# Performance work log

Measured on AMD Instinct MI355X. Metric: run time of the kernel, lower is better.

The kernel has to match this reference:

```python
import jax, jax.numpy as jnp
import numpy as np

J = 17  # coco joints
SKEL = ((1, 2), (0, 1), (0, 2), (2, 4), (1, 3), (6, 8), (8, 10), (5, 7), (7, 9),
        (12, 14), (14, 16), (11, 13), (13, 15), (5, 6), (11, 12), (5, 11), (6, 12), (3, 5), (4, 6))
EPS = 1e-5


def make_adj():
    a = np.eye(J, dtype=np.float32)
    for i, j in SKEL:
        a[i, j] = 1.0
        a[j, i] = 1.0
    return jnp.asarray(a)


def conv_block(feat, W, b, g, be, adj):
    # feat: [B,V,Din], W: [V,Din,Dout], b/g/be: [V,Dout]
    h = jnp.einsum('bvd,vdo->bvo', feat, W) + b
    # BatchNorm1d (training mode): per-vertex, per-channel batch stats (biased var)
    mu = h.mean(axis=0)
    var = h.var(axis=0)
    h = (h - mu) * jax.lax.rsqrt(var + EPS) * g + be
    h = jnp.einsum('vu,buo->bvo', adj, h)  # adjacency aggregation
    return jax.nn.relu(h)


def setup_inputs() -> dict:
    key = jax.random.key(0)
    ks = jax.random.split(key, 10)
    B, Din = 8192, 2048
    s0 = 1.0 / np.sqrt(Din)
    s1 = 1.0 / np.sqrt(J)
    img_feat = jax.random.normal(ks[0], (B, J, Din), dtype=jnp.float32)
    # first GraphConvBlock: 2048 -> 17, per-vertex params
    W0 = jax.random.uniform(ks[1], (J, Din, J), jnp.float32, -s0, s0)
    b0 = jax.random.uniform(ks[2], (J, J), jnp.float32, -s0, s0)
    g0 = jnp.ones((J, J), jnp.float32)
    be0 = jnp.zeros((J, J), jnp.float32)
    # 4 GraphResBlocks x 2 GraphConvBlocks = 8 blocks of dim 17 -> 17
    Wr = jax.random.uniform(ks[3], (8, J, J, J), jnp.float32, -s1, s1)
    br = jax.random.uniform(ks[4], (8, J, J), jnp.float32, -s1, s1)
    gr = jnp.ones((8, J, J), jnp.float32)
    ber = jnp.zeros((8, J, J), jnp.float32)
    return {"img_feat": img_feat, "W0": W0, "b0": b0, "g0": g0, "be0": be0,
            "Wr": Wr, "br": br, "gr": gr, "ber": ber}


def reference(img_feat, W0, b0, g0, be0, Wr, br, gr, ber):
    adj = make_adj()
    feat = conv_block(img_feat, W0, b0, g0, be0, adj)  # [B,17,17]
    for r in range(4):  # 4 GraphResBlocks
        i0, i1 = 2 * r, 2 * r + 1
        h = conv_block(feat, Wr[i0], br[i0], gr[i0], ber[i0], adj)
        h = conv_block(h, Wr[i1], br[i1], gr[i1], ber[i1], adj)
        feat = h + feat  # residual
    return feat
```

## Files before the change

kernel.cpp:

```cpp
#include <hip/hip_runtime.h>

#define J 17
#define JP 18
#define VO 289
#define NB 8192
#define DIN 2048
#define EPSB 1e-5f
#define KC 512
#define RT 32
#define NCH 68

typedef __attribute__((ext_vector_type(8))) short bf16x8;
typedef __attribute__((ext_vector_type(4))) float f32x4;
typedef __attribute__((ext_vector_type(4))) float f32x4v;

__device__ __constant__ unsigned ADJM[J] = {
  0x7u, 0xFu, 0x17u, 0x2Au, 0x54u, 0x8E8u, 0x1170u, 0x2A0u, 0x540u,
  0x280u, 0x500u, 0x3820u, 0x5840u, 0xA800u, 0x15000u, 0xA000u, 0x14000u};

__device__ inline unsigned short f2bf(float x){
  unsigned u = __float_as_uint(x);
  return (unsigned short)((u + 0x7fffu + ((u>>16)&1u)) >> 16);
}

__global__ void zero_stats(float* p, int n) {
  int i = blockIdx.x*blockDim.x + threadIdx.x;
  int stride = gridDim.x*blockDim.x;
  for (; i < n; i += stride) p[i] = 0.f;
}

__global__ __launch_bounds__(256) void wconv_kernel(
    const float* __restrict__ W0, unsigned short* __restrict__ Wp)
{
  int t = blockIdx.x*256 + threadIdx.x;
  int v = t >> 11, k = t & 2047;
  const float* src = W0 + (size_t)t*J;
  unsigned short* dst = Wp + (((size_t)v*256 + (k>>3))*17)*8 + (k&7);
  #pragma unroll
  for (int o=0;o<J;++o)  dst[o*8] = f2bf(src[o]);
}

__global__ __launch_bounds__(512) void conv0_kernel(
    const float* __restrict__ feat, const unsigned short* __restrict__ Wp,
    const float* __restrict__ b0, float* __restrict__ C,
    float* __restrict__ stat0)
{
  const int tid = threadIdx.x, w = tid>>6, l = tid&63;
  const int lo = l&15, oc = l>>4;
  const int sr = tid>>4, sc = tid&15;
  const int rowBase = blockIdx.x*RT;

  __shared__ __align__(16) unsigned short Ab[2][RT*KC];
  __shared__ float red[8][2][256];
  __shared__ float bS[VO], bQ[VO];

  for (int i=tid;i<VO;i+=512){ bS[i]=0.f; bQ[i]=0.f; }

  f32x4 acc00 = (f32x4){0.f,0.f,0.f,0.f};
  f32x4 acc01 = (f32x4){0.f,0.f,0.f,0.f};
  f32x4 acc10 = (f32x4){0.f,0.f,0.f,0.f};
  f32x4 acc11 = (f32x4){0.f,0.f,0.f,0.f};

  const float* frow = feat + (size_t)(rowBase + sr)*(J*DIN);
  f32x4v ld[8];

  auto issue = [&](int c){
    const f32x4v* src = (const f32x4v*)(frow + c*KC + sc*4);
    #pragma unroll
    for (int i=0;i<8;++i) ld[i] = __builtin_nontemporal_load(src + i*16);
  };
  auto writeLDS = [&](int buf){
    #pragma unroll
    for (int i=0;i<8;++i){
      ushort4 hv;
      hv.x=f2bf(ld[i].x); hv.y=f2bf(ld[i].y); hv.z=f2bf(ld[i].z); hv.w=f2bf(ld[i].w);
      const int f = sc*4 + i*64;
      *(ushort4*)&Ab[buf][(sr*KC + f) ^ ((sr&7)<<3)] = hv;
    }
  };

  issue(0); writeLDS(0);
  __syncthreads();

  const int swz = (lo&7)<<3;

  for (int c=0;c<NCH;++c){
    const int buf = c&1;
    if (c+1<NCH) issue(c+1);
    const int v = c>>2;
    #pragma unroll
    for (int ks=0;ks<2;++ks){
      const int kl = w*64 + ks*32 + oc*8;
      bf16x8 a0 = *(const bf16x8*)&Ab[buf][(lo*KC + kl) ^ swz];
      bf16x8 a1 = *(const bf16x8*)&Ab[buf][((16+lo)*KC + kl) ^ swz];
      const int kg8 = ((c&3)*KC + kl) >> 3;
      const unsigned short* fragBase = Wp + (((size_t)v*256 + kg8)*17)*8;
      bf16x8 bA = *(const bf16x8*)(fragBase + lo*8);
      bf16x8 bB = {0,0,0,0,0,0,0,0};
      if (lo==0) bB = *(const bf16x8*)(fragBase + 16*8);
      acc00 = __builtin_amdgcn_mfma_f32_16x16x32_bf16(a0, bA, acc00, 0,0,0);
      acc10 = __builtin_amdgcn_mfma_f32_16x16x32_bf16(a1, bA, acc10, 0,0,0);
      acc01 = __builtin_amdgcn_mfma_f32_16x16x32_bf16(a0, bB, acc01, 0,0,0);
      acc11 = __builtin_amdgcn_mfma_f32_16x16x32_bf16(a1, bB, acc11, 0,0,0);
    }
    if ((c&3)==3){
      #pragma unroll
      for (int pass=0; pass<2; ++pass){
        #pragma unroll
        for (int r=0;r<4;++r){
          red[w][0][(oc*4+r)*16+lo] = pass ? acc10[r] : acc00[r];
          red[w][1][(oc*4+r)*16+lo] = pass ? acc11[r] : acc01[r];
        }
        __syncthreads();
        if (tid < 256){
          const int er = tid>>4, ec = tid&15;
          const int ri = er*16+ec;
          float h0 = red[0][0][ri]+red[1][0][ri]+red[2][0][ri]+red[3][0][ri]
                   + red[4][0][ri]+red[5][0][ri]+red[6][0][ri]+red[7][0][ri]
                   + b0[v*J+ec];
          const int row = rowBase + pass*16 + er;
          C[(size_t)row*VO + v*J + ec] = h0;
          float s0 = h0, q0 = h0*h0;
          float s1 = 0.f, q1 = 0.f;
          if (ec==0){
            const int r2 = er*16;
            float h1 = red[0][1][r2]+red[1][1][r2]+red[2][1][r2]+red[3][1][r2]
                     + red[4][1][r2]+red[5][1][r2]+red[6][1][r2]+red[7][1][r2]
                     + b0[v*J+16];
            C[(size_t)row*VO + v*J + 16] = h1;
            s1 = h1; q1 = h1*h1;
          }
          s0 += __shfl_xor(s0,16); s0 += __shfl_xor(s0,32);
          q0 += __shfl_xor(q0,16); q0 += __shfl_xor(q0,32);
          s1 += __shfl_xor(s1,16); s1 += __shfl_xor(s1,32);
          q1 += __shfl_xor(q1,16); q1 += __shfl_xor(q1,32);
          if (l < 16){ atomicAdd(&bS[v*J+l], s0); atomicAdd(&bQ[v*J+l], q0); }
          if (l == 0){ atomicAdd(&bS[v*J+16], s1); atomicAdd(&bQ[v*J+16], q1); }
        }
        __syncthreads();
      }
      acc00 = (f32x4){0.f,0.f,0.f,0.f};
      acc01 = (f32x4){0.f,0.f,0.f,0.f};
      acc10 = (f32x4){0.f,0.f,0.f,0.f};
      acc11 = (f32x4){0.f,0.f,0.f,0.f};
    }
    if (c+1<NCH){
      writeLDS(buf^1);
      __syncthreads();
    }
  }

  __syncthreads();
  const int rep = blockIdx.x & 7;
  for (int i=tid;i<VO;i+=512){
    atomicAdd(&stat0[rep*512+i],        bS[i]);
    atomicAdd(&stat0[4096 + rep*512+i], bQ[i]);
  }
}

template<int RESID,int WRITEF,int CONV>
__global__ __launch_bounds__(256) void chain_kernel(
  const float* __restrict__ Cin, float* __restrict__ Cout,
  float* __restrict__ F,
  const float* __restrict__ statJ,
  const float* __restrict__ g, const float* __restrict__ be,
  const float* __restrict__ Wc, const float* __restrict__ bc,
  float* __restrict__ statN)
{
  __shared__ float wsmT[J*J*JP];
  __shared__ float bb[VO];
  __shared__ float aC[VO], cC[VO];
  __shared__ float hbX[4][2][J*JP];
  __shared__ float ssum[VO], ssq[VO];
  const int tid = threadIdx.x, wv = tid>>6, lane = tid&63;

  if (CONV) {
    for (int i=tid;i<J*J*J;i+=256) {
      int v = i/VO, rem = i - v*VO, d = rem/J, o = rem - d*J;
      wsmT[(v*J+o)*JP + d] = Wc[i];
    }
    for (int i=tid;i<VO;i+=256) bb[i]=bc[i];
  }
  for (int i=tid;i<VO;i+=256) {
    float s=0.f,q=0.f;
    #pragma unroll
    for (int r=0;r<8;++r){ s += statJ[r*512+i]; q += statJ[4096 + r*512+i]; }
    float mu  = s*(1.f/NB);
    float var = q*(1.f/NB) - mu*mu;
    float rs  = rsqrtf(var + EPSB);
    float A = rs*g[i];
    aC[i]=A; cC[i]=be[i]-mu*A;
    ssum[i]=0.f; ssq[i]=0.f;
  }
  __syncthreads();

  float sl[5]={0,0,0,0,0}, ql[5]={0,0,0,0,0};

  #pragma unroll
  for (int it=0; it<2; ++it) {
    const int r0 = blockIdx.x*16 + wv*4 + it*2;
    const float* c0 = Cin + (size_t)r0*VO;
    const float* c1 = c0 + VO;

    #pragma unroll
    for (int s=0;s<5;++s) {
      int vo = lane + 64*s;
      if (vo<VO) {
        int vtx = vo/J, o = vo - vtx*J;
        hbX[wv][0][vtx*JP+o] = c0[vo]*aC[vo] + cC[vo];
        hbX[wv][1][vtx*JP+o] = c1[vo]*aC[vo] + cC[vo];
      }
    }
    asm volatile("s_waitcnt lgkmcnt(0)" ::: "memory");

    float n0[5], n1[5];
    #pragma unroll
    for (int s=0;s<5;++s) {
      int vo = lane + 64*s;
      n0[s]=0.f; n1[s]=0.f;
      if (vo<VO) {
        int vtx = vo/J, o = vo - vtx*J;
        unsigned m = ADJM[vtx];
        float a0=0.f, a1=0.f;
        while (m) {
          int u = __ffs(m) - 1; m &= m-1;
          a0 += hbX[wv][0][u*JP+o];
          a1 += hbX[wv][1][u*JP+o];
        }
        a0 = a0>0.f?a0:0.f; a1 = a1>0.f?a1:0.f;
        size_t gi = (size_t)r0*VO + vo;
        if (RESID)  { a0 += F[gi]; a1 += F[gi+VO]; }
        if (WRITEF) { F[gi]=a0;    F[gi+VO]=a1; }
        n0[s]=a0; n1[s]=a1;
        if (!CONV) { Cout[gi]=a0; Cout[gi+VO]=a1; }
      }
    }

    if (CONV) {
      #pragma unroll
      for (int s=0;s<5;++s) {
        int vo = lane + 64*s;
        if (vo<VO) {
          int vtx = vo/J, o = vo - vtx*J;
          hbX[wv][0][vtx*JP+o] = n0[s];
          hbX[wv][1][vtx*JP+o] = n1[s];
        }
      }
      asm volatile("s_waitcnt lgkmcnt(0)" ::: "memory");
      #pragma unroll
      for (int s=0;s<5;++s) {
        int vo = lane + 64*s;
        if (vo<VO) {
          int vtx = vo/J, o = vo - vtx*J;
          const float* wp = &wsmT[(vtx*J+o)*JP];
          const float* h0 = &hbX[wv][0][vtx*JP];
          const float* h1 = &hbX[wv][1][vtx*JP];
          float a0 = bb[vo], a1 = a0;
          #pragma unroll
          for (int d=0;d<J;++d) {
            float w = wp[d];
            a0 += h0[d]*w; a1 += h1[d]*w;
          }
          size_t gi = (size_t)r0*VO + vo;
          Cout[gi]=a0; Cout[gi+VO]=a1;
          sl[s] += a0+a1; ql[s] += a0*a0 + a1*a1;
        }
      }
      asm volatile("s_waitcnt lgkmcnt(0)" ::: "memory");
    } else {
      asm volatile("s_waitcnt lgkmcnt(0)" ::: "memory");
    }
  }

  if (CONV) {
    #pragma unroll
    for (int s=0;s<5;++s) {
      int vo = lane + 64*s;
      if (vo<VO) { atomicAdd(&ssum[vo], sl[s]); atomicAdd(&ssq[vo], ql[s]); }
    }
    __syncthreads();
    const int rep = blockIdx.x & 7;
    for (int i=tid;i<VO;i+=256) {
      atomicAdd(&statN[rep*512+i],        ssum[i]);
      atomicAdd(&statN[4096 + rep*512+i], ssq[i]);
    }
  }
}

extern "C" void kernel_launch(void* const* d_in, const int* in_sizes, int n_in,
                              void* d_out, int out_size, void* d_ws, size_t ws_size,
                              hipStream_t stream)
{
  (void)in_sizes; (void)n_in; (void)out_size; (void)ws_size;
  const float* img = (const float*)d_in[0];
  const float* W0  = (const float*)d_in[1];
  const float* b0  = (const float*)d_in[2];
  const float* g0  = (const float*)d_in[3];
  const float* be0 = (const float*)d_in[4];
  const float* Wr  = (const float*)d_in[5];
  const float* br  = (const float*)d_in[6];
  const float* gr  = (const float*)d_in[7];
  const float* ber = (const float*)d_in[8];

  float* ws = (float*)d_ws;
  float* ST = ws;
  unsigned short* Wp = (unsigned short*)(ws + 73728);
  float* Ca = ws + 73728 + 300000;
  float* Cb = Ca + (size_t)NB*VO;
  float* F  = Cb + (size_t)NB*VO;
  float* out = (float*)d_out;

  zero_stats<<<72,256,0,stream>>>(ST, 9*8192);
  wconv_kernel<<<136,256,0,stream>>>(W0, Wp);

  conv0_kernel<<<256,512,0,stream>>>(img, Wp, b0, Ca, ST);

  const int W1 = J*J*J;
  #define STG(j) (ST + (j)*8192)
  chain_kernel<0,1,1><<<512,256,0,stream>>>(Ca, Cb, F, STG(0), g0,      be0,
                                            Wr+0*W1, br+0*VO, STG(1));
  chain_kernel<0,0,1><<<512,256,0,stream>>>(Cb, Ca, F, STG(1), gr+0*VO, ber+0*VO,
                                            Wr+1*W1, br+1*VO, STG(2));
  chain_kernel<1,1,1><<<512,256,0,stream>>>(Ca, Cb, F, STG(2), gr+1*VO, ber+1*VO,
                                            Wr+2*W1, br+2*VO, STG(3));
  chain_kernel<0,0,1><<<512,256,0,stream>>>(Cb, Ca, F, STG(3), gr+2*VO, ber+2*VO,
                                            Wr+3*W1, br+3*VO, STG(4));
  chain_kernel<1,1,1><<<512,256,0,stream>>>(Ca, Cb, F, STG(4), gr+3*VO, ber+3*VO,
                                            Wr+4*W1, br+4*VO, STG(5));
  chain_kernel<0,0,1><<<512,256,0,stream>>>(Cb, Ca, F, STG(5), gr+4*VO, ber+4*VO,
                                            Wr+5*W1, br+5*VO, STG(6));
  chain_kernel<1,1,1><<<512,256,0,stream>>>(Ca, Cb, F, STG(6), gr+5*VO, ber+5*VO,
                                            Wr+6*W1, br+6*VO, STG(7));
  chain_kernel<0,0,1><<<512,256,0,stream>>>(Cb, Ca, F, STG(7), gr+6*VO, ber+6*VO,
                                            Wr+7*W1, br+7*VO, STG(8));
  chain_kernel<1,0,0><<<512,256,0,stream>>>(Ca, out, F, STG(8), gr+7*VO, ber+7*VO,
                                            nullptr, nullptr, nullptr);
  #undef STG
}
```

Before: 431.3 us.

## Use bf16 MFMA for per-vertex 17x17 residual convs in chain kernel

Replaces the scalar fp32 per-vertex 17x17 matmul in the chain kernel with bf16 MFMA 16x16x32 instructions. The 16 rows of a block are staged as bf16 in a swizzled LDS buffer, and the weights are pre-packed into fragment layouts, with a second MFMA covering the 17th output channel. The intent is to cut the ALU cost of the small dense contractions and the per-row LDS traffic. In exchange, the residual-block activations and weights are rounded to bf16, which adds precision error, and most lanes of the second MFMA do wasted work.

```diff
diff --git a/kernel.cpp b/kernel.cpp
--- a/kernel.cpp
+++ b/kernel.cpp
@@ -167,123 +167,121 @@
   const float* __restrict__ Wc, const float* __restrict__ bc,
   float* __restrict__ statN)
 {
-  __shared__ float wsmT[J*J*JP];
-  __shared__ float bb[VO];
-  __shared__ float aC[VO], cC[VO];
-  __shared__ float hbX[4][2][J*JP];
+  __shared__ float aC[VO], cC[VO], bb[VO];
   __shared__ float ssum[VO], ssq[VO];
+  __shared__ float hb1[4][4][J*JP];
+  __shared__ __align__(16) unsigned short hb2[16*576];
+  __shared__ __align__(16) unsigned short wfA[17][64][8];
+  __shared__ __align__(16) unsigned short wfB[17][4][8];
+
   const int tid = threadIdx.x, wv = tid>>6, lane = tid&63;
-
-  if (CONV) {
-    for (int i=tid;i<J*J*J;i+=256) {
-      int v = i/VO, rem = i - v*VO, d = rem/J, o = rem - d*J;
-      wsmT[(v*J+o)*JP + d] = Wc[i];
-    }
-    for (int i=tid;i<VO;i+=256) bb[i]=bc[i];
-  }
-  for (int i=tid;i<VO;i+=256) {
+  const int lo = lane&15, oc = lane>>4;
+  const int rowBase = blockIdx.x*16;
+
+  for (int i=tid;i<VO;i+=256){
     float s=0.f,q=0.f;
     #pragma unroll
     for (int r=0;r<8;++r){ s += statJ[r*512+i]; q += statJ[4096 + r*512+i]; }
     float mu  = s*(1.f/NB);
     float var = q*(1.f/NB) - mu*mu;
-    float rs  = rsqrtf(var + EPSB);
-    float A = rs*g[i];
+    float A = rsqrtf(var + EPSB)*g[i];
     aC[i]=A; cC[i]=be[i]-mu*A;
     ssum[i]=0.f; ssq[i]=0.f;
-  }
-  __syncthreads();
-
-  float sl[5]={0,0,0,0,0}, ql[5]={0,0,0,0,0};
+    if (CONV) bb[i]=bc[i];
+  }
+  if (CONV){
+    for (int i=tid;i<16*576/8;i+=256) ((uint4*)hb2)[i] = (uint4){0,0,0,0};
+    for (int idx=tid; idx<17*64; idx+=256){
+      int v=idx>>6, ll=idx&63, c=ll&15, o8=ll>>4;
+      unsigned short* dst=&wfA[v][ll][0];
+      #pragma unroll
+      for (int j=0;j<8;++j){ int d=o8*8+j; dst[j] = (d<J)? f2bf(Wc[((size_t)v*J+d)*J+c]) : (unsigned short)0; }
+    }
+    for (int idx=tid; idx<17*4; idx+=256){
+      int v=idx>>2, o8=idx&3;
+      unsigned short* dst=&wfB[v][o8][0];
+      #pragma unroll
+      for (int j=0;j<8;++j){ int d=o8*8+j; dst[j] = (d<J)? f2bf(Wc[((size_t)v*J+d)*J+16]) : (unsigned short)0; }
+    }
+  }
+  __syncthreads();
 
   #pragma unroll
-  for (int it=0; it<2; ++it) {
-    const int r0 = blockIdx.x*16 + wv*4 + it*2;
-    const float* c0 = Cin + (size_t)r0*VO;
-    const float* c1 = c0 + VO;
-
-    #pragma unroll
-    for (int s=0;s<5;++s) {
+  for (int r4=0;r4<4;++r4){
+    const int row = wv*4 + r4;
+    const float* cr = Cin + (size_t)(rowBase+row)*VO;
+    #pragma unroll
+    for (int s=0;s<5;++s){
       int vo = lane + 64*s;
-      if (vo<VO) {
-        int vtx = vo/J, o = vo - vtx*J;
-        hbX[wv][0][vtx*JP+o] = c0[vo]*aC[vo] + cC[vo];
-        hbX[wv][1][vtx*JP+o] = c1[vo]*aC[vo] + cC[vo];
-      }
-    }
-    asm volatile("s_waitcnt lgkmcnt(0)" ::: "memory");
-
-    float n0[5], n1[5];
-    #pragma unroll
-    for (int s=0;s<5;++s) {
+      if (vo<VO){ int vtx=vo/J, o=vo-vtx*J; hb1[wv][r4][vtx*JP+o] = cr[vo]*aC[vo] + cC[vo]; }
+    }
+  }
+  asm volatile("s_waitcnt lgkmcnt(0)" ::: "memory");
+  #pragma unroll
+  for (int r4=0;r4<4;++r4){
+    const int row = wv*4 + r4;
+    #pragma unroll
+    for (int s=0;s<5;++s){
       int vo = lane + 64*s;
-      n0[s]=0.f; n1[s]=0.f;
-      if (vo<VO) {
-        int vtx = vo/J, o = vo - vtx*J;
+      if (vo<VO){
+        int vtx=vo/J, o=vo-vtx*J;
         unsigned m = ADJM[vtx];
-        float a0=0.f, a1=0.f;
-        while (m) {
-          int u = __ffs(m) - 1; m &= m-1;
-          a0 += hbX[wv][0][u*JP+o];
-          a1 += hbX[wv][1][u*JP+o];
-        }
-        a0 = a0>0.f?a0:0.f; a1 = a1>0.f?a1:0.f;
-        size_t gi = (size_t)r0*VO + vo;
-        if (RESID)  { a0 += F[gi]; a1 += F[gi+VO]; }
-        if (WRITEF) { F[gi]=a0;    F[gi+VO]=a1; }
-        n0[s]=a0; n1[s]=a1;
-        if (!CONV) { Cout[gi]=a0; Cout[gi+VO]=a1; }
-      }
-    }
-
-    if (CONV) {
-      #pragma unroll
-      for (int s=0;s<5;++s) {
-        int vo = lane + 64*s;
-        if (vo<VO) {
-          int vtx = vo/J, o = vo - vtx*J;
-          hbX[wv][0][vtx*JP+o] = n0[s];
-          hbX[wv][1][vtx*JP+o] = n1[s];
+        float a = 0.f;
+        while (m){ int u=__ffs(m)-1; m&=m-1; a += hb1[wv][r4][u*JP+o]; }
+        a = a>0.f ? a : 0.f;
+        size_t gi = (size_t)(rowBase+row)*VO + vo;
+        if (RESID)  a += F[gi];
+        if (WRITEF) F[gi] = a;
+        if (CONV){
+          int idx = (row*576 + vtx*32 + o) ^ ((row&7)<<3);
+          hb2[idx] = f2bf(a);
+        } else {
+          Cout[gi] = a;
         }
       }
-      asm volatile("s_waitcnt lgkmcnt(0)" ::: "memory");
-      #pragma unroll
-      for (int s=0;s<5;++s) {
-        int vo = lane + 64*s;
-        if (vo<VO) {
-          int vtx = vo/J, o = vo - vtx*J;
-          const float* wp = &wsmT[(vtx*J+o)*JP];
-          const float* h0 = &hbX[wv][0][vtx*JP];
-          const float* h1 = &hbX[wv][1][vtx*JP];
-          float a0 = bb[vo], a1 = a0;
-          #pragma unroll
-          for (int d=0;d<J;++d) {
-            float w = wp[d];
-            a0 += h0[d]*w; a1 += h1[d]*w;
-          }
-          size_t gi = (size_t)r0*VO + vo;
-          Cout[gi]=a0; Cout[gi+VO]=a1;
-          sl[s] += a0+a1; ql[s] += a0*a0 + a1*a1;
-        }
+    }
+  }
+  if (!CONV) return;
+  __syncthreads();
+
+  for (int v=wv; v<J; v+=4){
+    const int aidx = (lo*576 + v*32 + oc*8) ^ ((lo&7)<<3);
+    bf16x8 a  = *(const bf16x8*)&hb2[aidx];
+    bf16x8 bA = *(const bf16x8*)&wfA[v][lane][0];
+    bf16x8 bB = {0,0,0,0,0,0,0,0};
+    if (lo==0) bB = *(const bf16x8*)&wfB[v][oc][0];
+    f32x4 acc0 = (f32x4){0.f,0.f,0.f,0.f};
+    f32x4 acc1 = (f32x4){0.f,0.f,0.f,0.f};
+    acc0 = __builtin_amdgcn_mfma_f32_16x16x32_bf16(a, bA, acc0, 0,0,0);
+    acc1 = __builtin_amdgcn_mfma_f32_16x16x32_bf16(a, bB, acc1, 0,0,0);
+
+    const float bias0 = bb[v*J+lo];
+    const float bias1 = bb[v*J+16];
+    float s0=0.f,q0=0.f,s1=0.f,q1=0.f;
+    #pragma unroll
+    for (int r=0;r<4;++r){
+      const int row = rowBase + oc*4 + r;
+      const float h0 = acc0[r] + bias0;
+      Cout[(size_t)row*VO + v*J + lo] = h0;
+      s0 += h0; q0 += h0*h0;
+      if (lo==0){
+        const float h1 = acc1[r] + bias1;
+        Cout[(size_t)row*VO + v*J + 16] = h1;
+        s1 += h1; q1 += h1*h1;
       }
-      asm volatile("s_waitcnt lgkmcnt(0)" ::: "memory");
-    } else {
-      asm volatile("s_waitcnt lgkmcnt(0)" ::: "memory");
-    }
-  }
-
-  if (CONV) {
-    #pragma unroll
-    for (int s=0;s<5;++s) {
-      int vo = lane + 64*s;
-      if (vo<VO) { atomicAdd(&ssum[vo], sl[s]); atomicAdd(&ssq[vo], ql[s]); }
-    }
-    __syncthreads();
-    const int rep = blockIdx.x & 7;
-    for (int i=tid;i<VO;i+=256) {
-      atomicAdd(&statN[rep*512+i],        ssum[i]);
-      atomicAdd(&statN[4096 + rep*512+i], ssq[i]);
-    }
+    }
+    s0 += __shfl_xor(s0,16); s0 += __shfl_xor(s0,32);
+    q0 += __shfl_xor(q0,16); q0 += __shfl_xor(q0,32);
+    s1 += __shfl_xor(s1,16); s1 += __shfl_xor(s1,32);
+    q1 += __shfl_xor(q1,16); q1 += __shfl_xor(q1,32);
+    if (lane < 16){ atomicAdd(&ssum[v*J+lo], s0); atomicAdd(&ssq[v*J+lo], q0); }
+    if (lane == 0){ atomicAdd(&ssum[v*J+16], s1); atomicAdd(&ssq[v*J+16], q1); }
+  }
+  __syncthreads();
+  const int rep = blockIdx.x & 7;
+  for (int i=tid;i<VO;i+=256){
+    atomicAdd(&statN[rep*512+i],        ssum[i]);
+    atomicAdd(&statN[4096 + rep*512+i], ssq[i]);
   }
 }
 
```

Result: slower. 471.8 us (+9.4%).
